# Kernel optimization log

Hardware: AMD Instinct MI355X
Metric: run time of the kernel (lower is better)

Reference implementation:

```python
import jax, jax.numpy as jnp
import numpy as np

NU, NI = 16384, 8192          # num_users, num_items
DK, DM = 64, 64               # embed_k, embed_k_multimod
DV, DT = 4096, 384            # visual / textual feature dims
TOP_K = 10
N_LAYERS = 1                  # item-graph propagation layers
N_UI_LAYERS = 2               # user-item LGConv layers
L_M = 0.7
E = 524288                    # user-item interactions (doubled to symmetric edges)


def build_sim(x):
    # cosine similarity: row-normalize then x @ x.T  -> [N, N]
    xn = x / jnp.linalg.norm(x, axis=-1, keepdims=True)
    return xn @ xn.T


def build_knn(sim, k):
    # keep top-k values per row, zero elsewhere (torch topk + scatter_)
    vals, idx = jax.lax.top_k(sim, k)
    rows = jnp.arange(sim.shape[0])[:, None]
    return jnp.zeros_like(sim).at[rows, idx].set(vals)


def normalized_laplacian(adj):
    # D^{-1/2} A D^{-1/2}; inf (zero-degree) -> 0, applied as row/col scaling
    d = adj.sum(-1)
    dis = jnp.where(d > 0, jax.lax.rsqrt(jnp.where(d > 0, d, 1.0)), 0.0)
    return adj * dis[:, None] * dis[None, :]


def l2_normalize(x, axis=-1, eps=1e-12):
    n = jnp.linalg.norm(x, axis=axis, keepdims=True)
    return x / jnp.maximum(n, eps)


def setup_inputs() -> dict:
    key = jax.random.key(0)
    ks = jax.random.split(key, 8)
    Gu = jax.random.normal(ks[0], (NU, DK), jnp.float32) * 0.1
    Gi = jax.random.normal(ks[1], (NI, DK), jnp.float32) * 0.1
    feat_v = jax.random.normal(ks[2], (NI, DV), jnp.float32)
    feat_t = jax.random.normal(ks[3], (NI, DT), jnp.float32)
    W_v = jax.random.normal(ks[4], (DV, DM), jnp.float32) / np.sqrt(DV)
    b_v = jnp.zeros((DM,), jnp.float32)
    W_t = jax.random.normal(ks[5], (DT, DM), jnp.float32) / np.sqrt(DT)
    b_t = jnp.zeros((DM,), jnp.float32)
    importance_weights = jnp.full((2,), 0.5, jnp.float32)
    # precomputed per-modality normalized laplacians from raw (detached) features
    Sim_v = normalized_laplacian(build_knn(build_sim(feat_v), TOP_K))
    Sim_t = normalized_laplacian(build_knn(build_sim(feat_t), TOP_K))
    # symmetric bipartite user-item edge list (items offset by NU)
    u = jax.random.randint(ks[6], (E,), 0, NU)
    i = jax.random.randint(ks[7], (E,), 0, NI) + NU
    edge_index = jnp.stack([jnp.concatenate([u, i]), jnp.concatenate([i, u])])
    return dict(Gu=Gu, Gi=Gi, feat_v=feat_v, feat_t=feat_t, W_v=W_v, b_v=b_v,
                W_t=W_t, b_t=b_t, importance_weights=importance_weights,
                Sim_v=Sim_v, Sim_t=Sim_t, edge_index=edge_index)


def propagate(Gu, Gi, feat_v, feat_t, W_v, b_v, W_t, b_t,
              importance_weights, Sim_v, Sim_t, edge_index):
    w = jax.nn.softmax(importance_weights)
    learned = jnp.zeros((NI, NI), jnp.float32)
    original = jnp.zeros((NI, NI), jnp.float32)
    for m, (feat, W, b, Sim) in enumerate(
            [(feat_v, W_v, b_v, Sim_v), (feat_t, W_t, b_t, Sim_t)]):
        proj = feat @ W + b                                  # [NI, DM]
        learned = learned + w[m] * build_knn(build_sim(proj), TOP_K)
        original = original + w[m] * Sim
    Si = (1.0 - L_M) * normalized_laplacian(learned) + L_M * original
    # item-graph propagation
    item_emb = Gi
    for _ in range(N_LAYERS):
        item_emb = Si @ item_emb                              # [NI, DK]
    # user-item LGConv (normalize=False => plain sum aggregation)
    src, dst = edge_index[0], edge_index[1]
    all_emb = [jnp.concatenate([Gu, Gi], 0)]                  # [NU+NI, DK]
    for _ in range(N_UI_LAYERS):
        agg = jax.ops.segment_sum(all_emb[-1][src], dst, num_segments=NU + NI)
        all_emb.append(l2_normalize(agg, axis=1))
    mean_emb = jnp.stack(all_emb, 1).mean(1)
    gu, gi = mean_emb[:NU], mean_emb[NU:]
    return gu, gi + l2_normalize(item_emb, axis=1)


def reference(Gu, Gi, feat_v, feat_t, W_v, b_v, W_t, b_t,
              importance_weights, Sim_v, Sim_t, edge_index):
    return propagate(Gu, Gi, feat_v, feat_t, W_v, b_v, W_t, b_t,
                     importance_weights, Sim_v, Sim_t, edge_index)
```

## Files before the change

kernel.cpp:

```cpp
#include <hip/hip_runtime.h>
#include <hip/hip_bf16.h>

#define NU 16384
#define NI 8192
#define TOPK 10
#define NTOT (NU + NI)
#define OCAP 64
#define NSEG 4
#define CSEG (NI / NSEG)
#define NGRP 512
#define MAXSEL 16

typedef short short8v __attribute__((ext_vector_type(8)));
typedef float float4v __attribute__((ext_vector_type(4)));

__device__ __forceinline__ float warp64_sum(float v) {
#pragma unroll
  for (int m = 32; m >= 1; m >>= 1) v += __shfl_xor(v, m);
  return v;
}

__device__ __forceinline__ unsigned int umap(float f) {
  unsigned int b = __float_as_uint(f);
  return b ^ ((b & 0x80000000u) ? 0xFFFFFFFFu : 0x80000000u);
}

__global__ __launch_bounds__(256) void proj_partial_kernel(
    const float* __restrict__ feat, const float* __restrict__ W,
    float* __restrict__ partial, int D, int kchunk) {
  __shared__ float sA[64][64];
  __shared__ float sB[64][68];
  const int tid = threadIdx.x;
  const int r0 = blockIdx.x * 64;
  const int ks = blockIdx.y;
  const int rg = tid >> 4, cg = tid & 15;
  const int rA = tid & 63, kgA = (tid >> 6) * 16;
  const int kB = tid & 63, cbB = (tid >> 6) * 16;
  const int kbeg = ks * kchunk, kend = kbeg + kchunk;
  float4 pa[4], pb[4];
  {
    const float* fp = feat + (size_t)(r0 + rA) * D + kbeg + kgA;
    pa[0] = *(const float4*)(fp + 0);  pa[1] = *(const float4*)(fp + 4);
    pa[2] = *(const float4*)(fp + 8);  pa[3] = *(const float4*)(fp + 12);
    const float* wp = W + (size_t)(kbeg + kB) * 64 + cbB;
    pb[0] = *(const float4*)(wp + 0);  pb[1] = *(const float4*)(wp + 4);
    pb[2] = *(const float4*)(wp + 8);  pb[3] = *(const float4*)(wp + 12);
  }
  float acc[4][4] = {{0,0,0,0},{0,0,0,0},{0,0,0,0},{0,0,0,0}};
  for (int kc = kbeg; kc < kend; kc += 64) {
#pragma unroll
    for (int i = 0; i < 4; ++i) {
      sA[kgA + 4*i + 0][rA] = pa[i].x;
      sA[kgA + 4*i + 1][rA] = pa[i].y;
      sA[kgA + 4*i + 2][rA] = pa[i].z;
      sA[kgA + 4*i + 3][rA] = pa[i].w;
      *(float4*)&sB[kB][cbB + 4*i] = pb[i];
    }
    __syncthreads();
    if (kc + 64 < kend) {
      const float* fp = feat + (size_t)(r0 + rA) * D + kc + 64 + kgA;
      pa[0] = *(const float4*)(fp + 0);  pa[1] = *(const float4*)(fp + 4);
      pa[2] = *(const float4*)(fp + 8);  pa[3] = *(const float4*)(fp + 12);
      const float* wp = W + (size_t)(kc + 64 + kB) * 64 + cbB;
      pb[0] = *(const float4*)(wp + 0);  pb[1] = *(const float4*)(wp + 4);
      pb[2] = *(const float4*)(wp + 8);  pb[3] = *(const float4*)(wp + 12);
    }
#pragma unroll 8
    for (int k = 0; k < 64; ++k) {
      float4 a = *(const float4*)&sA[k][rg * 4];
      float4 b = *(const float4*)&sB[k][cg * 4];
      acc[0][0] += a.x * b.x; acc[0][1] += a.x * b.y; acc[0][2] += a.x * b.z; acc[0][3] += a.x * b.w;
      acc[1][0] += a.y * b.x; acc[1][1] += a.y * b.y; acc[1][2] += a.y * b.z; acc[1][3] += a.y * b.w;
      acc[2][0] += a.z * b.x; acc[2][1] += a.z * b.y; acc[2][2] += a.z * b.z; acc[2][3] += a.z * b.w;
      acc[3][0] += a.w * b.x; acc[3][1] += a.w * b.y; acc[3][2] += a.w * b.z; acc[3][3] += a.w * b.w;
    }
    __syncthreads();
  }
#pragma unroll
  for (int rr = 0; rr < 4; ++rr) {
    float4 o = make_float4(acc[rr][0], acc[rr][1], acc[rr][2], acc[rr][3]);
    *(float4*)(partial + ((size_t)ks * NI + r0 + rg * 4 + rr) * 64 + cg * 4) = o;
  }
}

__global__ __launch_bounds__(256) void proj_reduce_kernel(
    const float* __restrict__ partial, const float* __restrict__ b, int ksplit,
    float* __restrict__ xn, ushort* __restrict__ hi, ushort* __restrict__ lo) {
  const int row = blockIdx.x * 4 + (threadIdx.x >> 6);
  const int col = threadIdx.x & 63;
  float acc = b[col];
  for (int ks = 0; ks < ksplit; ++ks)
    acc += partial[((size_t)ks * NI + row) * 64 + col];
  float ss = warp64_sum(acc * acc);
  float v = acc * (1.0f / sqrtf(ss));
  xn[(size_t)row * 64 + col] = v;
  __hip_bfloat16 hb = __float2bfloat16(v);
  float hf = __bfloat162float(hb);
  __hip_bfloat16 lb = __float2bfloat16(v - hf);
  hi[(size_t)row * 64 + col] = *(ushort*)&hb;
  lo[(size_t)row * 64 + col] = *(ushort*)&lb;
}

__global__ __launch_bounds__(256) void sim_tilemax_kernel(
    const ushort* __restrict__ hiV, const ushort* __restrict__ loV,
    const ushort* __restrict__ hiT, const ushort* __restrict__ loT,
    float* __restrict__ tmax) {
  const int m = blockIdx.z;
  const ushort* hi = m ? hiT : hiV;
  const ushort* lo = m ? loT : loV;
  const int seg = blockIdx.y;
  const int c_base = seg * CSEG;
  const int r_base = blockIdx.x * 64;
  __shared__ ushort sH[64][64];
  __shared__ ushort sL[64][64];
  const int tid = threadIdx.x;
  const int wave = tid >> 6, lane = tid & 63;
  const int lr = lane & 15, lg = lane >> 4;
  const int my_row = r_base + wave * 16 + lr;
  short8v bh[2], bl[2];
  {
    const ushort* rp = hi + (size_t)my_row * 64 + lg * 8;
    bh[0] = *(const short8v*)(rp);
    bh[1] = *(const short8v*)(rp + 32);
    const ushort* rp2 = lo + (size_t)my_row * 64 + lg * 8;
    bl[0] = *(const short8v*)(rp2);
    bl[1] = *(const short8v*)(rp2 + 32);
  }
  float* tbase = tmax + ((size_t)m * NI + my_row) * NGRP + seg * (CSEG / 16);

  const int sc = tid >> 2, sq = (tid & 3) * 32;
  const int sw = (sc & 7) << 4;
  for (int c0 = 0; c0 < CSEG; c0 += 64) {
    __syncthreads();
    const char* gh = (const char*)(hi + (size_t)(c_base + c0 + sc) * 64);
    const char* gl2 = (const char*)(lo + (size_t)(c_base + c0 + sc) * 64);
    *(float4*)((char*)&sH[sc][0] + (sq ^ sw)) = *(const float4*)(gh + sq);
    *(float4*)((char*)&sH[sc][0] + ((sq + 16) ^ sw)) = *(const float4*)(gh + sq + 16);
    *(float4*)((char*)&sL[sc][0] + (sq ^ sw)) = *(const float4*)(gl2 + sq);
    *(float4*)((char*)&sL[sc][0] + ((sq + 16) ^ sw)) = *(const float4*)(gl2 + sq + 16);
    __syncthreads();
#pragma unroll
    for (int s = 0; s < 4; ++s) {
      const int ca = s * 16 + lr;
      const int cw = (ca & 7) << 4;
      const int kb0 = (lg * 16) ^ cw;
      const int kb1 = (lg * 16 + 64) ^ cw;
      short8v ah0 = *(const short8v*)((const char*)&sH[ca][0] + kb0);
      short8v ah1 = *(const short8v*)((const char*)&sH[ca][0] + kb1);
      short8v al0 = *(const short8v*)((const char*)&sL[ca][0] + kb0);
      short8v al1 = *(const short8v*)((const char*)&sL[ca][0] + kb1);
      float4v acc = {0.f, 0.f, 0.f, 0.f};
      acc = __builtin_amdgcn_mfma_f32_16x16x32_bf16(ah0, bh[0], acc, 0, 0, 0);
      acc = __builtin_amdgcn_mfma_f32_16x16x32_bf16(ah1, bh[1], acc, 0, 0, 0);
      acc = __builtin_amdgcn_mfma_f32_16x16x32_bf16(ah0, bl[0], acc, 0, 0, 0);
      acc = __builtin_amdgcn_mfma_f32_16x16x32_bf16(ah1, bl[1], acc, 0, 0, 0);
      acc = __builtin_amdgcn_mfma_f32_16x16x32_bf16(al0, bh[0], acc, 0, 0, 0);
      acc = __builtin_amdgcn_mfma_f32_16x16x32_bf16(al1, bh[1], acc, 0, 0, 0);
      float gm = fmaxf(fmaxf(acc[0], acc[1]), fmaxf(acc[2], acc[3]));
      gm = fmaxf(gm, __shfl_xor(gm, 16));
      gm = fmaxf(gm, __shfl_xor(gm, 32));
      if (lg == 0) tbase[(c0 >> 4) + s] = gm;
    }
  }
}

__global__ __launch_bounds__(256) void tile_rescore_kernel(
    const float* __restrict__ xn_v, const float* __restrict__ xn_t,
    const float* __restrict__ tmax,
    float* __restrict__ tkvV, int* __restrict__ tkiV,
    float* __restrict__ tkvT, int* __restrict__ tkiT) {
  const int bid = blockIdx.x;
  const int m = bid >> 13;
  const int row = bid & (NI - 1);
  const float* xn = m ? xn_t : xn_v;
  const int tid = threadIdx.x;
  __shared__ int ssel[MAXSEL];
  __shared__ float sval[MAXSEL * 16];
  __shared__ int scol[MAXSEL * 16];
  __shared__ float lv[32];
  __shared__ int lc[32];
  __shared__ int lnum;
  const int grp = tid >> 4, l16 = tid & 15;
  float4 rq = ((const float4*)(xn + (size_t)row * 64))[l16];
  if (tid < 64) {
    const int lane = tid;
    const float4* tmr4 = (const float4*)(tmax + ((size_t)m * NI + row) * NGRP);
    float4 t0 = tmr4[lane];
    float4 t1 = tmr4[64 + lane];
    unsigned int uv[8] = {umap(t0.x), umap(t0.y), umap(t0.z), umap(t0.w),
                          umap(t1.x), umap(t1.y), umap(t1.z), umap(t1.w)};
    unsigned long long blo = 0, bhi = 0x100000000ull;
    unsigned int taub = 0;
    for (int it = 0; it < 34; ++it) {
      unsigned int mid = (unsigned int)((blo + bhi) >> 1);
      int cnt = 0;
#pragma unroll
      for (int j = 0; j < 8; ++j) cnt += __popcll(__ballot(uv[j] >= mid));
      if (cnt >= 12) {
        taub = mid;
        if (cnt <= MAXSEL) break;
        blo = (unsigned long long)mid + 1;
      } else {
        bhi = mid;
      }
      if (blo >= bhi) break;
    }
    unsigned long long bj[8];
    int base[8];
    int tot = 0;
#pragma unroll
    for (int j = 0; j < 8; ++j) {
      bj[j] = __ballot(uv[j] >= taub);
      base[j] = tot;
      tot += __popcll(bj[j]);
    }
    if (lane < MAXSEL) ssel[lane] = -1;
    unsigned long long ltm = (1ull << lane) - 1ull;
#pragma unroll
    for (int j = 0; j < 8; ++j) {
      if (uv[j] >= taub) {
        int pos = base[j] + __popcll(bj[j] & ltm);
        if (pos < MAXSEL) {
          int g = (j < 4) ? (lane * 4 + j) : (256 + lane * 4 + (j - 4));
          ssel[pos] = g;
        }
      }
    }
  }
  __syncthreads();
  for (int it = 0; it < MAXSEL; ++it) {
    int gsel = ssel[it];
    bool valid = (gsel >= 0);
    int c = valid ? (gsel * 16 + grp) : 0;
    float4 x4 = ((const float4*)(xn + (size_t)c * 64))[l16];
    float s = rq.x * x4.x + rq.y * x4.y + rq.z * x4.z + rq.w * x4.w;
    s += __shfl_xor(s, 1);
    s += __shfl_xor(s, 2);
    s += __shfl_xor(s, 4);
    s += __shfl_xor(s, 8);
    if (l16 == 0) {
      sval[it * 16 + grp] = valid ? s : -3.0e38f;
      scol[it * 16 + grp] = valid ? c : 0x7fffffff;
    }
  }
  __syncthreads();
  if (tid < 64) {
    const int lane = tid;
    float fv[4];
    int fc[4];
    unsigned int uv4[4];
#pragma unroll
    for (int k = 0; k < 4; ++k) {
      fv[k] = sval[lane + 64 * k];
      fc[k] = scol[lane + 64 * k];
      uv4[k] = umap(fv[k]);
    }
    unsigned long long blo = 0, bhi = 0x100000000ull;
    unsigned int taub = 0;
    for (int it = 0; it < 34; ++it) {
      unsigned int mid = (unsigned int)((blo + bhi) >> 1);
      int cnt = 0;
#pragma unroll
      for (int k = 0; k < 4; ++k) cnt += __popcll(__ballot(uv4[k] >= mid));
      if (cnt >= TOPK) {
        taub = mid;
        if (cnt == TOPK) break;
        blo = (unsigned long long)mid + 1;
      } else {
        bhi = mid;
      }
      if (blo >= bhi) break;
    }
    unsigned long long bk[4];
    int base[4];
    int tot = 0;
#pragma unroll
    for (int k = 0; k < 4; ++k) {
      bk[k] = __ballot(uv4[k] >= taub);
      base[k] = tot;
      tot += __popcll(bk[k]);
    }
    float* tv = m ? tkvT : tkvV;
    int* ti = m ? tkiT : tkiV;
    unsigned long long ltm = (1ull << lane) - 1ull;
    if (tot == TOPK) {
#pragma unroll
      for (int k = 0; k < 4; ++k) {
        if (uv4[k] >= taub) {
          int pos = base[k] + __popcll(bk[k] & ltm);
          tv[(size_t)row * TOPK + pos] = fv[k];
          ti[(size_t)row * TOPK + pos] = fc[k];
        }
      }
    } else {
#pragma unroll
      for (int k = 0; k < 4; ++k) {
        if (uv4[k] >= taub) {
          int pos = base[k] + __popcll(bk[k] & ltm);
          if (pos < 32) { lv[pos] = fv[k]; lc[pos] = fc[k]; }
        }
      }
      if (lane == 0) lnum = (tot < 32) ? tot : 32;
      if (lane == 0) {
        int n = lnum;
        unsigned int used = 0;
        for (int q = 0; q < TOPK; ++q) {
          float bv = -3.0e38f;
          int bc = 0x7fffffff, bi = -1;
          for (int i2 = 0; i2 < n; ++i2) {
            if (used & (1u << i2)) continue;
            if (lv[i2] > bv || (lv[i2] == bv && lc[i2] < bc)) {
              bv = lv[i2]; bc = lc[i2]; bi = i2;
            }
          }
          used |= (1u << bi);
          tv[(size_t)row * TOPK + q] = bv;
          ti[(size_t)row * TOPK + q] = bc;
        }
      }
    }
  }
}

__global__ void dis_kernel(const float* __restrict__ tkv_v, const float* __restrict__ tkv_t,
                           const float* __restrict__ iw, float* __restrict__ dis) {
  int r = blockIdx.x * blockDim.x + threadIdx.x;
  if (r >= NI) return;
  float ea = expf(iw[0]), eb = expf(iw[1]);
  float w0 = ea / (ea + eb), w1 = eb / (ea + eb);
  float s0 = 0.f, s1 = 0.f;
  for (int j = 0; j < TOPK; ++j) { s0 += tkv_v[r * TOPK + j]; s1 += tkv_t[r * TOPK + j]; }
  float d = w0 * s0 + w1 * s1;
  dis[r] = (d > 0.0f) ? (1.0f / sqrtf(d)) : 0.0f;
}

__global__ __launch_bounds__(256) void scan_sim_kernel(
    const float* __restrict__ Sv, const float* __restrict__ St,
    const float* __restrict__ iw, int* __restrict__ ocols,
    float* __restrict__ ow, int* __restrict__ ocnt) {
  const int lane = threadIdx.x & 63;
  const int row = blockIdx.x * 4 + (threadIdx.x >> 6);
  float ea = expf(iw[0]), eb = expf(iw[1]);
  float wA = 0.7f * ea / (ea + eb), wB = 0.7f * eb / (ea + eb);
  int cnt = 0;
  int* oc = ocols + (size_t)row * OCAP;
  float* op = ow + (size_t)row * OCAP;
#pragma unroll 1
  for (int m = 0; m < 2; ++m) {
    const float* S = m ? St : Sv;
    float wgt = m ? wB : wA;
    const float4* rp = (const float4*)(S + (size_t)row * NI);
    for (int it = 0; it < NI / 256; ++it) {
      float4 v = rp[it * 64 + lane];
      int cb = it * 256 + lane * 4;
#pragma unroll
      for (int j = 0; j < 4; ++j) {
        float x = (j == 0) ? v.x : (j == 1) ? v.y : (j == 2) ? v.z : v.w;
        bool nz = (x != 0.0f);
        unsigned long long mk = __ballot(nz);
        int pre = __popcll(mk & ((1ull << lane) - 1ull));
        if (nz) {
          int p = cnt + pre;
          if (p < OCAP) { oc[p] = cb + j; op[p] = wgt * x; }
        }
        cnt += __popcll(mk);
      }
    }
  }
  if (lane == 0) ocnt[row] = (cnt < OCAP) ? cnt : OCAP;
}

__global__ __launch_bounds__(256) void item_emb_kernel(
    const float* __restrict__ Gi,
    const float* __restrict__ tkv_v, const int* __restrict__ tki_v,
    const float* __restrict__ tkv_t, const int* __restrict__ tki_t,
    const float* __restrict__ dis, const int* __restrict__ ocols,
    const float* __restrict__ ow, const int* __restrict__ ocnt,
    const float* __restrict__ iw, float* __restrict__ nitem) {
  const int d = threadIdx.x & 63;
  const int row = blockIdx.x * 4 + (threadIdx.x >> 6);
  float ea = expf(iw[0]), eb = expf(iw[1]);
  float w0 = ea / (ea + eb), w1 = eb / (ea + eb);
  float disr = dis[row];
  float acc = 0.0f;
#pragma unroll 1
  for (int m = 0; m < 2; ++m) {
    const float* tv = m ? tkv_t : tkv_v;
    const int* ti = m ? tki_t : tki_v;
    float wm = (m ? w1 : w0) * 0.3f * disr;
    for (int j = 0; j < TOPK; ++j) {
      float val = tv[(size_t)row * TOPK + j];
      int c = ti[(size_t)row * TOPK + j];
      acc += wm * val * dis[c] * Gi[(size_t)c * 64 + d];
    }
  }
  int cn = ocnt[row];
  for (int j = 0; j < cn; ++j) {
    int c = ocols[(size_t)row * OCAP + j];
    float wv = ow[(size_t)row * OCAP + j];
    acc += wv * Gi[(size_t)c * 64 + d];
  }
  float ss = warp64_sum(acc * acc);
  float nr = sqrtf(ss);
  nitem[(size_t)row * 64 + d] = acc / fmaxf(nr, 1e-12f);
}

__global__ void hist_kernel(const int* __restrict__ dst, int* __restrict__ deg, int n) {
  int e = blockIdx.x * blockDim.x + threadIdx.x;
  if (e < n) atomicAdd(&deg[dst[e]], 1);
}

__global__ __launch_bounds__(256) void scanA_kernel(
    const int* __restrict__ deg, int* __restrict__ loc, int* __restrict__ bsum) {
  __shared__ int s[256];
  int tid = threadIdx.x, gid = blockIdx.x * 256 + tid;
  int x = deg[gid];
  s[tid] = x;
  __syncthreads();
  for (int off = 1; off < 256; off <<= 1) {
    int t = (tid >= off) ? s[tid - off] : 0;
    __syncthreads();
    s[tid] += t;
    __syncthreads();
  }
  loc[gid] = s[tid] - x;
  if (tid == 255) bsum[blockIdx.x] = s[255];
}

__global__ __launch_bounds__(256) void scanC_kernel(
    const int* __restrict__ loc, const int* __restrict__ bsum,
    int* __restrict__ row_ptr, int* __restrict__ cursor, int n) {
  int gid = blockIdx.x * blockDim.x + threadIdx.x;
  if (gid > n) return;
  int blk = gid >> 8;
  int off = 0;
  for (int b2 = 0; b2 < blk; ++b2) off += bsum[b2];
  if (gid == n) { row_ptr[n] = off; return; }
  int v = off + loc[gid];
  row_ptr[gid] = v;
  cursor[gid] = v;
}

__global__ void fill_kernel(const int* __restrict__ src, const int* __restrict__ dst,
                            int* __restrict__ cursor, int* __restrict__ csr, int n) {
  int e = blockIdx.x * blockDim.x + threadIdx.x;
  if (e < n) {
    int p = atomicAdd(&cursor[dst[e]], 1);
    csr[p] = src[e];
  }
}

__global__ __launch_bounds__(256) void segsum_kernel(
    const float* __restrict__ inU, const float* __restrict__ inI,
    const int* __restrict__ row_ptr, const int* __restrict__ csr,
    float* __restrict__ outp) {
  const int d = threadIdx.x & 63;
  const int row = blockIdx.x * 4 + (threadIdx.x >> 6);
  int a = row_ptr[row], bnd = row_ptr[row + 1];
  float acc = 0.0f;
  for (int e = a; e < bnd; ++e) {
    int s = csr[e];
    const float* sp = (s < NU) ? (inU + (size_t)s * 64) : (inI + (size_t)(s - NU) * 64);
    acc += sp[d];
  }
  float ss = warp64_sum(acc * acc);
  float nr = sqrtf(ss);
  outp[(size_t)row * 64 + d] = acc / fmaxf(nr, 1e-12f);
}

__global__ __launch_bounds__(256) void segsum_final_kernel(
    const float* __restrict__ e1b, const int* __restrict__ row_ptr,
    const int* __restrict__ csr, const float* __restrict__ Gu,
    const float* __restrict__ Gi, const float* __restrict__ nitem,
    float* __restrict__ outp) {
  const int d = threadIdx.x & 63;
  const int row = blockIdx.x * 4 + (threadIdx.x >> 6);
  const float* inU = e1b;
  const float* inI = e1b + (size_t)NU * 64;
  int a = row_ptr[row], bnd = row_ptr[row + 1];
  float acc = 0.0f;
  for (int e = a; e < bnd; ++e) {
    int s = csr[e];
    const float* sp = (s < NU) ? (inU + (size_t)s * 64) : (inI + (size_t)(s - NU) * 64);
    acc += sp[d];
  }
  float ss = warp64_sum(acc * acc);
  float e2 = acc / fmaxf(sqrtf(ss), 1e-12f);
  float base = (row < NU) ? Gu[(size_t)row * 64 + d] : Gi[(size_t)(row - NU) * 64 + d];
  float v = (base + e1b[(size_t)row * 64 + d] + e2) * (1.0f / 3.0f);
  if (row >= NU) v += nitem[(size_t)(row - NU) * 64 + d];
  outp[(size_t)row * 64 + d] = v;
}

extern "C" void kernel_launch(void* const* d_in, const int* in_sizes, int n_in,
                              void* d_out, int out_size, void* d_ws, size_t ws_size,
                              hipStream_t stream) {
  const float* Gu = (const float*)d_in[0];
  const float* Gi = (const float*)d_in[1];
  const float* feat_v = (const float*)d_in[2];
  const float* feat_t = (const float*)d_in[3];
  const float* W_v = (const float*)d_in[4];
  const float* b_v = (const float*)d_in[5];
  const float* W_t = (const float*)d_in[6];
  const float* b_t = (const float*)d_in[7];
  const float* iw = (const float*)d_in[8];
  const float* Sv = (const float*)d_in[9];
  const float* St = (const float*)d_in[10];
  const int* eidx = (const int*)d_in[11];
  const int twoE = in_sizes[11] / 2;
  const int* esrc = eidx;
  const int* edst = eidx + twoE;
  float* outp = (float*)d_out;

  char* w = (char*)d_ws;
  size_t off = 0;
  auto alloc = [&](size_t bytes) -> void* {
    void* p = w + off;
    off = (off + bytes + 255) & ~(size_t)255;
    return p;
  };
  float* xn_v = (float*)alloc((size_t)NI * 64 * 4);
  float* xn_t = (float*)alloc((size_t)NI * 64 * 4);
  ushort* hiV = (ushort*)alloc((size_t)NI * 64 * 2);
  ushort* loV = (ushort*)alloc((size_t)NI * 64 * 2);
  ushort* hiT = (ushort*)alloc((size_t)NI * 64 * 2);
  ushort* loT = (ushort*)alloc((size_t)NI * 64 * 2);
  float* tmax = (float*)alloc((size_t)2 * NI * NGRP * 4);
  float* tkvV = (float*)alloc((size_t)NI * TOPK * 4);
  int* tkiV = (int*)alloc((size_t)NI * TOPK * 4);
  float* tkvT = (float*)alloc((size_t)NI * TOPK * 4);
  int* tkiT = (int*)alloc((size_t)NI * TOPK * 4);
  float* dis = (float*)alloc((size_t)NI * 4);
  int* ocols = (int*)alloc((size_t)NI * OCAP * 4);
  float* ow = (float*)alloc((size_t)NI * OCAP * 4);
  int* ocnt = (int*)alloc((size_t)NI * 4);
  float* nitem = (float*)alloc((size_t)NI * 64 * 4);
  float* e1b = (float*)alloc((size_t)NTOT * 64 * 4);
  int* deg = (int*)alloc((size_t)NTOT * 4);
  int* row_ptr = (int*)alloc((size_t)(NTOT + 1) * 4);
  int* cursor = (int*)alloc((size_t)NTOT * 4);
  int* csr = (int*)alloc((size_t)twoE * 4);
  int* locb = (int*)alloc((size_t)NTOT * 4);
  int* bsum = (int*)alloc((size_t)(NTOT / 256) * 4);
  if (off > ws_size) return;

  float* partial = tmax;

  hipMemsetAsync(deg, 0, (size_t)NTOT * 4, stream);

  proj_partial_kernel<<<dim3(NI / 64, 8), 256, 0, stream>>>(feat_v, W_v, partial, 4096, 512);
  proj_reduce_kernel<<<NI / 4, 256, 0, stream>>>(partial, b_v, 8, xn_v, hiV, loV);
  proj_partial_kernel<<<dim3(NI / 64, 6), 256, 0, stream>>>(feat_t, W_t, partial, 384, 64);
  proj_reduce_kernel<<<NI / 4, 256, 0, stream>>>(partial, b_t, 6, xn_t, hiT, loT);
  sim_tilemax_kernel<<<dim3(NI / 64, NSEG, 2), 256, 0, stream>>>(hiV, loV, hiT, loT, tmax);
  tile_rescore_kernel<<<2 * NI, 256, 0, stream>>>(xn_v, xn_t, tmax, tkvV, tkiV,
                                                  tkvT, tkiT);
  dis_kernel<<<(NI + 255) / 256, 256, 0, stream>>>(tkvV, tkvT, iw, dis);
  scan_sim_kernel<<<NI / 4, 256, 0, stream>>>(Sv, St, iw, ocols, ow, ocnt);
  item_emb_kernel<<<NI / 4, 256, 0, stream>>>(Gi, tkvV, tkiV, tkvT, tkiT, dis, ocols, ow,
                                              ocnt, iw, nitem);
  hist_kernel<<<(twoE + 255) / 256, 256, 0, stream>>>(edst, deg, twoE);
  scanA_kernel<<<NTOT / 256, 256, 0, stream>>>(deg, locb, bsum);
  scanC_kernel<<<(NTOT + 1 + 255) / 256, 256, 0, stream>>>(locb, bsum, row_ptr, cursor, NTOT);
  fill_kernel<<<(twoE + 255) / 256, 256, 0, stream>>>(esrc, edst, cursor, csr, twoE);
  segsum_kernel<<<NTOT / 4, 256, 0, stream>>>(Gu, Gi, row_ptr, csr, e1b);
  segsum_final_kernel<<<NTOT / 4, 256, 0, stream>>>(e1b, row_ptr, csr, Gu, Gi, nitem, outp);
}
```

Baseline: 693.3 us.

## Merge independent stages into combined launches via block-index partitioning

Puts the edge degree histogram inside the visual projection launch, and runs the sparse Laplacian scan, the similarity tile-max and the CSR fill together in one launch. Each block picks its role from its index. The scans of the degree prefix are moved ahead so the fill can share the launch. The goal is to cut launch count and let memory-bound and compute-bound work overlap on the GPU. The cost is a larger register and LDS footprint for every block, which may lower occupancy for the lighter roles.

```diff
diff --git a/kernel.cpp b/kernel.cpp
--- a/kernel.cpp
+++ b/kernel.cpp
@@ -23,6 +23,71 @@
 __device__ __forceinline__ unsigned int umap(float f) {
   unsigned int b = __float_as_uint(f);
   return b ^ ((b & 0x80000000u) ? 0xFFFFFFFFu : 0x80000000u);
+}
+
+__global__ __launch_bounds__(256) void fused_proj_hist_kernel(
+    const float* __restrict__ feat, const float* __restrict__ W,
+    float* __restrict__ partial, int D, int kchunk,
+    const int* __restrict__ dst, int* __restrict__ deg, int nedge) {
+  __shared__ float sA[64][64];
+  __shared__ float sB[64][68];
+  const int tid = threadIdx.x;
+  if (blockIdx.x < 4096) {
+    int e = blockIdx.x * 256 + tid;
+    if (e < nedge) atomicAdd(&deg[dst[e]], 1);
+    return;
+  }
+  const int pb = blockIdx.x - 4096;
+  const int r0 = (pb & 127) * 64;
+  const int ks = pb >> 7;
+  const int rg = tid >> 4, cg = tid & 15;
+  const int rA = tid & 63, kgA = (tid >> 6) * 16;
+  const int kB = tid & 63, cbB = (tid >> 6) * 16;
+  const int kbeg = ks * kchunk, kend = kbeg + kchunk;
+  float4 pa[4], pb4[4];
+  {
+    const float* fp = feat + (size_t)(r0 + rA) * D + kbeg + kgA;
+    pa[0] = *(const float4*)(fp + 0);  pa[1] = *(const float4*)(fp + 4);
+    pa[2] = *(const float4*)(fp + 8);  pa[3] = *(const float4*)(fp + 12);
+    const float* wp = W + (size_t)(kbeg + kB) * 64 + cbB;
+    pb4[0] = *(const float4*)(wp + 0);  pb4[1] = *(const float4*)(wp + 4);
+    pb4[2] = *(const float4*)(wp + 8);  pb4[3] = *(const float4*)(wp + 12);
+  }
+  float acc[4][4] = {{0,0,0,0},{0,0,0,0},{0,0,0,0},{0,0,0,0}};
+  for (int kc = kbeg; kc < kend; kc += 64) {
+#pragma unroll
+    for (int i = 0; i < 4; ++i) {
+      sA[kgA + 4*i + 0][rA] = pa[i].x;
+      sA[kgA + 4*i + 1][rA] = pa[i].y;
+      sA[kgA + 4*i + 2][rA] = pa[i].z;
+      sA[kgA + 4*i + 3][rA] = pa[i].w;
+      *(float4*)&sB[kB][cbB + 4*i] = pb4[i];
+    }
+    __syncthreads();
+    if (kc + 64 < kend) {
+      const float* fp = feat + (size_t)(r0 + rA) * D + kc + 64 + kgA;
+      pa[0] = *(const float4*)(fp + 0);  pa[1] = *(const float4*)(fp + 4);
+      pa[2] = *(const float4*)(fp + 8);  pa[3] = *(const float4*)(fp + 12);
+      const float* wp = W + (size_t)(kc + 64 + kB) * 64 + cbB;
+      pb4[0] = *(const float4*)(wp + 0);  pb4[1] = *(const float4*)(wp + 4);
+      pb4[2] = *(const float4*)(wp + 8);  pb4[3] = *(const float4*)(wp + 12);
+    }
+#pragma unroll 8
+    for (int k = 0; k < 64; ++k) {
+      float4 a = *(const float4*)&sA[k][rg * 4];
+      float4 b = *(const float4*)&sB[k][cg * 4];
+      acc[0][0] += a.x * b.x; acc[0][1] += a.x * b.y; acc[0][2] += a.x * b.z; acc[0][3] += a.x * b.w;
+      acc[1][0] += a.y * b.x; acc[1][1] += a.y * b.y; acc[1][2] += a.y * b.z; acc[1][3] += a.y * b.w;
+      acc[2][0] += a.z * b.x; acc[2][1] += a.z * b.y; acc[2][2] += a.z * b.z; acc[2][3] += a.z * b.w;
+      acc[3][0] += a.w * b.x; acc[3][1] += a.w * b.y; acc[3][2] += a.w * b.z; acc[3][3] += a.w * b.w;
+    }
+    __syncthreads();
+  }
+#pragma unroll
+  for (int rr = 0; rr < 4; ++rr) {
+    float4 o = make_float4(acc[rr][0], acc[rr][1], acc[rr][2], acc[rr][3]);
+    *(float4*)(partial + ((size_t)ks * NI + r0 + rg * 4 + rr) * 64 + cg * 4) = o;
+  }
 }
 
 __global__ __launch_bounds__(256) void proj_partial_kernel(
@@ -101,19 +166,68 @@
   lo[(size_t)row * 64 + col] = *(ushort*)&lb;
 }
 
-__global__ __launch_bounds__(256) void sim_tilemax_kernel(
+__global__ __launch_bounds__(256) void fused_sim_kernel(
+    const float* __restrict__ Sv, const float* __restrict__ St,
+    const float* __restrict__ iw, int* __restrict__ ocols,
+    float* __restrict__ ow, int* __restrict__ ocnt,
     const ushort* __restrict__ hiV, const ushort* __restrict__ loV,
     const ushort* __restrict__ hiT, const ushort* __restrict__ loT,
-    float* __restrict__ tmax) {
-  const int m = blockIdx.z;
-  const ushort* hi = m ? hiT : hiV;
-  const ushort* lo = m ? loT : loV;
-  const int seg = blockIdx.y;
-  const int c_base = seg * CSEG;
-  const int r_base = blockIdx.x * 64;
+    float* __restrict__ tmax,
+    const int* __restrict__ esrc, const int* __restrict__ edst,
+    int* __restrict__ cursor, int* __restrict__ csr, int nedge) {
   __shared__ ushort sH[64][64];
   __shared__ ushort sL[64][64];
   const int tid = threadIdx.x;
+  const int bid = blockIdx.x;
+  if (bid < 2048) {
+    const int lane = tid & 63;
+    const int row = bid * 4 + (tid >> 6);
+    float ea = expf(iw[0]), eb = expf(iw[1]);
+    float wA = 0.7f * ea / (ea + eb), wB = 0.7f * eb / (ea + eb);
+    int cnt = 0;
+    int* oc = ocols + (size_t)row * OCAP;
+    float* op = ow + (size_t)row * OCAP;
+#pragma unroll 1
+    for (int m = 0; m < 2; ++m) {
+      const float* S = m ? St : Sv;
+      float wgt = m ? wB : wA;
+      const float4* rp = (const float4*)(S + (size_t)row * NI);
+      for (int it = 0; it < NI / 256; ++it) {
+        float4 v = rp[it * 64 + lane];
+        int cb = it * 256 + lane * 4;
+#pragma unroll
+        for (int j = 0; j < 4; ++j) {
+          float x = (j == 0) ? v.x : (j == 1) ? v.y : (j == 2) ? v.z : v.w;
+          bool nz = (x != 0.0f);
+          unsigned long long mk = __ballot(nz);
+          int pre = __popcll(mk & ((1ull << lane) - 1ull));
+          if (nz) {
+            int p = cnt + pre;
+            if (p < OCAP) { oc[p] = cb + j; op[p] = wgt * x; }
+          }
+          cnt += __popcll(mk);
+        }
+      }
+    }
+    if (lane == 0) ocnt[row] = (cnt < OCAP) ? cnt : OCAP;
+    return;
+  }
+  if (bid >= 3072) {
+    int e = (bid - 3072) * 256 + tid;
+    if (e < nedge) {
+      int p = atomicAdd(&cursor[edst[e]], 1);
+      csr[p] = esrc[e];
+    }
+    return;
+  }
+  const int t2 = bid - 2048;
+  const int m = t2 >> 9;
+  const int rest = t2 & 511;
+  const int seg = rest >> 7;
+  const int r_base = (rest & 127) * 64;
+  const ushort* hi = m ? hiT : hiV;
+  const ushort* lo = m ? loT : loV;
+  const int c_base = seg * CSEG;
   const int wave = tid >> 6, lane = tid & 63;
   const int lr = lane & 15, lg = lane >> 4;
   const int my_row = r_base + wave * 16 + lr;
@@ -127,7 +241,6 @@
     bl[1] = *(const short8v*)(rp2 + 32);
   }
   float* tbase = tmax + ((size_t)m * NI + my_row) * NGRP + seg * (CSEG / 16);
-
   const int sc = tid >> 2, sq = (tid & 3) * 32;
   const int sw = (sc & 7) << 4;
   for (int c0 = 0; c0 < CSEG; c0 += 64) {
@@ -334,42 +447,6 @@
   dis[r] = (d > 0.0f) ? (1.0f / sqrtf(d)) : 0.0f;
 }
 
-__global__ __launch_bounds__(256) void scan_sim_kernel(
-    const float* __restrict__ Sv, const float* __restrict__ St,
-    const float* __restrict__ iw, int* __restrict__ ocols,
-    float* __restrict__ ow, int* __restrict__ ocnt) {
-  const int lane = threadIdx.x & 63;
-  const int row = blockIdx.x * 4 + (threadIdx.x >> 6);
-  float ea = expf(iw[0]), eb = expf(iw[1]);
-  float wA = 0.7f * ea / (ea + eb), wB = 0.7f * eb / (ea + eb);
-  int cnt = 0;
-  int* oc = ocols + (size_t)row * OCAP;
-  float* op = ow + (size_t)row * OCAP;
-#pragma unroll 1
-  for (int m = 0; m < 2; ++m) {
-    const float* S = m ? St : Sv;
-    float wgt = m ? wB : wA;
-    const float4* rp = (const float4*)(S + (size_t)row * NI);
-    for (int it = 0; it < NI / 256; ++it) {
-      float4 v = rp[it * 64 + lane];
-      int cb = it * 256 + lane * 4;
-#pragma unroll
-      for (int j = 0; j < 4; ++j) {
-        float x = (j == 0) ? v.x : (j == 1) ? v.y : (j == 2) ? v.z : v.w;
-        bool nz = (x != 0.0f);
-        unsigned long long mk = __ballot(nz);
-        int pre = __popcll(mk & ((1ull << lane) - 1ull));
-        if (nz) {
-          int p = cnt + pre;
-          if (p < OCAP) { oc[p] = cb + j; op[p] = wgt * x; }
-        }
-        cnt += __popcll(mk);
-      }
-    }
-  }
-  if (lane == 0) ocnt[row] = (cnt < OCAP) ? cnt : OCAP;
-}
-
 __global__ __launch_bounds__(256) void item_emb_kernel(
     const float* __restrict__ Gi,
     const float* __restrict__ tkv_v, const int* __restrict__ tki_v,
@@ -405,11 +482,6 @@
   nitem[(size_t)row * 64 + d] = acc / fmaxf(nr, 1e-12f);
 }
 
-__global__ void hist_kernel(const int* __restrict__ dst, int* __restrict__ deg, int n) {
-  int e = blockIdx.x * blockDim.x + threadIdx.x;
-  if (e < n) atomicAdd(&deg[dst[e]], 1);
-}
-
 __global__ __launch_bounds__(256) void scanA_kernel(
     const int* __restrict__ deg, int* __restrict__ loc, int* __restrict__ bsum) {
   __shared__ int s[256];
@@ -439,15 +511,6 @@
   int v = off + loc[gid];
   row_ptr[gid] = v;
   cursor[gid] = v;
-}
-
-__global__ void fill_kernel(const int* __restrict__ src, const int* __restrict__ dst,
-                            int* __restrict__ cursor, int* __restrict__ csr, int n) {
-  int e = blockIdx.x * blockDim.x + threadIdx.x;
-  if (e < n) {
-    int p = atomicAdd(&cursor[dst[e]], 1);
-    csr[p] = src[e];
-  }
 }
 
 __global__ __launch_bounds__(256) void segsum_kernel(
@@ -548,21 +611,21 @@
 
   hipMemsetAsync(deg, 0, (size_t)NTOT * 4, stream);
 
-  proj_partial_kernel<<<dim3(NI / 64, 8), 256, 0, stream>>>(feat_v, W_v, partial, 4096, 512);
+  fused_proj_hist_kernel<<<4096 + 1024, 256, 0, stream>>>(
+      feat_v, W_v, partial, 4096, 512, edst, deg, twoE);
   proj_reduce_kernel<<<NI / 4, 256, 0, stream>>>(partial, b_v, 8, xn_v, hiV, loV);
   proj_partial_kernel<<<dim3(NI / 64, 6), 256, 0, stream>>>(feat_t, W_t, partial, 384, 64);
   proj_reduce_kernel<<<NI / 4, 256, 0, stream>>>(partial, b_t, 6, xn_t, hiT, loT);
-  sim_tilemax_kernel<<<dim3(NI / 64, NSEG, 2), 256, 0, stream>>>(hiV, loV, hiT, loT, tmax);
+  scanA_kernel<<<NTOT / 256, 256, 0, stream>>>(deg, locb, bsum);
+  scanC_kernel<<<(NTOT + 1 + 255) / 256, 256, 0, stream>>>(locb, bsum, row_ptr, cursor, NTOT);
+  fused_sim_kernel<<<2048 + 1024 + 4096, 256, 0, stream>>>(
+      Sv, St, iw, ocols, ow, ocnt, hiV, loV, hiT, loT, tmax,
+      esrc, edst, cursor, csr, twoE);
   tile_rescore_kernel<<<2 * NI, 256, 0, stream>>>(xn_v, xn_t, tmax, tkvV, tkiV,
                                                   tkvT, tkiT);
   dis_kernel<<<(NI + 255) / 256, 256, 0, stream>>>(tkvV, tkvT, iw, dis);
-  scan_sim_kernel<<<NI / 4, 256, 0, stream>>>(Sv, St, iw, ocols, ow, ocnt);
   item_emb_kernel<<<NI / 4, 256, 0, stream>>>(Gi, tkvV, tkiV, tkvT, tkiT, dis, ocols, ow,
                                               ocnt, iw, nitem);
-  hist_kernel<<<(twoE + 255) / 256, 256, 0, stream>>>(edst, deg, twoE);
-  scanA_kernel<<<NTOT / 256, 256, 0, stream>>>(deg, locb, bsum);
-  scanC_kernel<<<(NTOT + 1 + 255) / 256, 256, 0, stream>>>(locb, bsum, row_ptr, cursor, NTOT);
-  fill_kernel<<<(twoE + 255) / 256, 256, 0, stream>>>(esrc, edst, cursor, csr, twoE);
   segsum_kernel<<<NTOT / 4, 256, 0, stream>>>(Gu, Gi, row_ptr, csr, e1b);
   segsum_final_kernel<<<NTOT / 4, 256, 0, stream>>>(e1b, row_ptr, csr, Gu, Gi, nitem, outp);
 }
```

After: 673.7 us. -2.8%, faster.
